# Kernel optimization log

Measured on AMD Instinct MI355X. Metric: run time of the kernel, lower is better.

Reference implementation:

```python
import jax, jax.numpy as jnp
import numpy as np
import math

EPS = 1e-6

def _std(x, axis=None, keepdims=False):
    # torch.std default: unbiased (ddof=1)
    return jnp.std(x, axis=axis, keepdims=keepdims, ddof=1)

def setup_inputs() -> dict:
    key = jax.random.key(0)
    L = 2048
    inputs = jax.random.normal(key, (L,), dtype=jnp.float32)
    return {"inputs": inputs, "freq": 7}

def reference(inputs, freq):
    L = inputs.shape[0]
    t = jnp.linspace(-1.0, 1.0, L)
    phi = (2.0 * math.pi * freq) * t  # [L]

    # ---- coarse Lattice Lock search over 10x20x20x20 Gielis topologies ----
    m_grid = jnp.arange(1, 11, dtype=jnp.float32)             # [10]
    n1_grid = jnp.logspace(-1.0, 1.0, 20)                      # [20]
    n2_grid = jnp.logspace(-1.0, 1.0, 20)
    n3_grid = jnp.logspace(-1.0, 1.0, 20)

    M = m_grid[:, None, None, None, None]
    N1 = n1_grid[None, :, None, None, None]
    N2 = n2_grid[None, None, :, None, None]
    N3 = n3_grid[None, None, None, :, None]
    P = phi[None, None, None, None, :]                          # [1,1,1,1,L]

    # Gielis superformula projection: R = (|cos(m*phi/4)|^n2 + |sin(m*phi/4)|^n3)^(-1/n1)
    ang = M * P / 4.0                                           # [10,1,1,1,L] -> bcast
    ghost = (jnp.abs(jnp.cos(ang)) ** N2 + jnp.abs(jnp.sin(ang)) ** N3) ** (-1.0 / N1)
    ghost = ghost * jnp.sin(P)                                  # [10,20,20,20,L]
    ghost = (ghost - ghost.mean(-1, keepdims=True)) / (_std(ghost, -1, True) + EPS)

    target = (inputs - inputs.mean()) / (_std(inputs) + EPS)    # [L]

    mse = jnp.mean((ghost - target) ** 2, axis=-1)              # [10,20,20,20]
    mi, i1, i2, i3 = jnp.unravel_index(jnp.argmin(mse), mse.shape)
    c_m = m_grid[mi]
    c_n1 = n1_grid[i1]
    c_n2 = n2_grid[i2]
    c_n3 = n3_grid[i3]

    # ---- fine search 30x30x30 around coarse optimum (m fixed) ----
    n1_f = jnp.linspace(c_n1 * 0.8, c_n1 * 1.2, 30)
    n2_f = jnp.linspace(c_n2 * 0.8, c_n2 * 1.2, 30)
    n3_f = jnp.linspace(c_n3 * 0.8, c_n3 * 1.2, 30)
    N1_F = n1_f[:, None, None, None]
    N2_F = n2_f[None, :, None, None]
    N3_F = n3_f[None, None, :, None]
    PHI_F = phi[None, None, None, :]

    ang_f = c_m * PHI_F / 4.0
    R_f = (jnp.abs(jnp.cos(ang_f)) ** N2_F + jnp.abs(jnp.sin(ang_f)) ** N3_F) ** (-1.0 / N1_F)
    S_f = R_f * jnp.sin(PHI_F)                                  # [30,30,30,L]
    S_f = (S_f - S_f.mean(-1, keepdims=True)) / (_std(S_f, -1, True) + EPS)

    mse_f = jnp.mean((S_f - target) ** 2, axis=-1)              # [30,30,30]
    f1, f2, f3 = jnp.unravel_index(jnp.argmin(mse_f), mse_f.shape)

    return jnp.stack([c_m, n1_f[f1], n2_f[f2], n3_f[f3]])
```

## Files before the change

### kernel.cpp

```cpp
#include <hip/hip_runtime.h>

#define L    2048
#define HALF 1024
#define NM   10
#define NG   20
#define NF   30

#define NCC2 2000
#define NFC2 450

#define OFF_SC   0
#define OFF_TAB  2048
#define OFF_G20  (2048 + 2*NM*HALF)
#define OFF_R20  (OFF_G20 + 20)
#define OFF_DWS  (OFF_R20 + 20)

#define EXP2F(x) __builtin_amdgcn_exp2f(x)
#define LOG2F(x) __builtin_amdgcn_logf(x)

typedef float f32x2 __attribute__((ext_vector_type(2)));

__device__ __forceinline__ f32x2 pk_mul(f32x2 a, f32x2 b) { return a * b; }
__device__ __forceinline__ f32x2 pk_fma(f32x2 a, f32x2 b, f32x2 c) {
  return __builtin_elementwise_fma(a, b, c);
}
__device__ __forceinline__ f32x2 pk_exp2(f32x2 v) {
  f32x2 e; e.x = EXP2F(v.x); e.y = EXP2F(v.y); return e;
}

__device__ __forceinline__ float grid20(int i) {
  double e = -1.0 + 2.0 * (double)i / 19.0;
  return (float)exp2(e * 3.3219280948873623478703194294894);
}
__device__ __forceinline__ float finev(float c, int j) {
  return (float)((double)c * 0.8 + (double)j * ((double)c * 0.4 / 29.0));
}
__device__ __forceinline__ double mse_from(double sgg2, double sgt, double sum_tt) {
  double S = sgg2; if (S < 0.0) S = 0.0;
  double d = sqrt(S / (double)(L - 1)) + 1e-6;
  return (S / (d * d) - 2.0 * sgt / d + sum_tt) / (double)L;
}
__device__ __forceinline__ void vt_wave_reduce(double& v, int& t) {
  for (int o = 32; o > 0; o >>= 1) {
    double ov = __shfl_down(v, o);
    int ot = __shfl_down(t, o);
    if (ov < v || (ov == v && ot < t)) { v = ov; t = ot; }
  }
}
__device__ __forceinline__ void vt_block_merge(double& v, int& t, double* sv, int* st) {
  int lane = threadIdx.x & 63, w = threadIdx.x >> 6;
  vt_wave_reduce(v, t);
  if (lane == 0) { sv[w] = v; st[w] = t; }
  __syncthreads();
  if (threadIdx.x == 0) {
    for (int k = 1; k < 4; k++)
      if (sv[k] < v || (sv[k] == v && st[k] < t)) { v = sv[k]; t = st[k]; }
  }
}

__global__ __launch_bounds__(256) void k_init(const float* __restrict__ x,
                                              const int* __restrict__ freqp,
                                              float* __restrict__ fws,
                                              double* __restrict__ dstt) {
  if (blockIdx.x == 0) {
    int tid = threadIdx.x;
    int lane = tid & 63, w = tid >> 6;
    __shared__ double sh[8];
    __shared__ double s_mean, s_d;

    double sx = 0.0, sxx = 0.0;
    for (int l = tid; l < L; l += 256) {
      double v = (double)x[l];
      sx += v; sxx += v * v;
    }
    for (int o = 32; o > 0; o >>= 1) { sx += __shfl_down(sx, o); sxx += __shfl_down(sxx, o); }
    if (lane == 0) { sh[w] = sx; sh[4 + w] = sxx; }
    __syncthreads();
    if (tid == 0) {
      sx = sh[0] + sh[1] + sh[2] + sh[3];
      sxx = sh[4] + sh[5] + sh[6] + sh[7];
      double mean = sx / (double)L;
      double S = sxx - sx * sx / (double)L; if (S < 0.0) S = 0.0;
      s_mean = mean; s_d = sqrt(S / (double)(L - 1)) + 1e-6;
    }
    __syncthreads();
    double mean = s_mean, d = s_d;
    double freq = (double)freqp[0];

    double stt = 0.0;
    for (int l = tid; l < HALF; l += 256) {
      float tva = (float)(((double)x[l] - mean) / d);
      float tvb = (float)(((double)x[L - 1 - l] - mean) / d);
      float tdv = tva - tvb;
      double t = -1.0 + 2.0 * (double)l / 2047.0;
      float spv = (float)sin(6.2831853071795864769 * freq * t);
      float2 scv; scv.x = spv * spv; scv.y = spv * tdv;
      reinterpret_cast<float2*>(fws + OFF_SC)[l] = scv;
      stt += (double)tva * (double)tva + (double)tvb * (double)tvb;
    }
    for (int o = 32; o > 0; o >>= 1) { stt += __shfl_down(stt, o); }
    __syncthreads();
    if (lane == 0) { sh[w] = stt; }
    __syncthreads();
    if (tid == 0) { dstt[0] = sh[0] + sh[1] + sh[2] + sh[3]; }
  } else {
    int l = (blockIdx.x - 1) * 256 + threadIdx.x;
    double freq = (double)freqp[0];
    double t = -1.0 + 2.0 * (double)l / 2047.0;
    double theta = 6.2831853071795864769 * freq * t * 0.25;
    double s1, c1;
    sincos(theta, &s1, &c1);
    double sk = s1, ck = c1;
    float2* tabp = reinterpret_cast<float2*>(fws + OFF_TAB);
#pragma unroll
    for (int m = 0; m < NM; ++m) {
      float2 v;
      v.x = fmaxf(LOG2F(fabsf((float)ck)), -1.0e4f);
      v.y = fmaxf(LOG2F(fabsf((float)sk)), -1.0e4f);
      tabp[m * HALF + l] = v;
      double sn = sk * c1 + ck * s1;
      double cn = ck * c1 - sk * s1;
      sk = sn; ck = cn;
    }
    if (blockIdx.x == 1 && threadIdx.x < NG) {
      float g = grid20(threadIdx.x);
      fws[OFF_G20 + threadIdx.x] = g;
      fws[OFF_R20 + threadIdx.x] = -1.0f / g;
    }
  }
}

__global__ __launch_bounds__(256) void k_coarse(const float* __restrict__ fws,
                                                const double* __restrict__ dstt,
                                                double* __restrict__ bv,
                                                int* __restrict__ bt) {
  __shared__ float4 row_ls[512];
  __shared__ float4 row_sc[512];
  __shared__ float2 cells[40];
  __shared__ int cellt[40];
  int tid = threadIdx.x, lane = tid & 63, w = tid >> 6;
  int b = blockIdx.x;
  int m = b / 200;
  int rem = b % 200;
  int i2 = rem / 10;
  int p3 = rem % 10;
  int i3A = 2 * p3;
  float n2 = fws[OFF_G20 + i2];
  float n3A = fws[OFF_G20 + i3A];
  float n3B = fws[OFF_G20 + i3A + 1];

  const float2* tab = reinterpret_cast<const float2*>(fws + OFF_TAB) + m * HALF;
  const float2* sc = reinterpret_cast<const float2*>(fws + OFF_SC);
#pragma unroll
  for (int k = 0; k < 2; k++) {
    int q = tid + k * 256;
    int e0 = 2 * q, e1 = e0 + 1;
    float2 tb0 = tab[e0], tb1 = tab[e1];
    float2 s0 = sc[e0], s1 = sc[e1];
    float a20 = EXP2F(n2 * tb0.x), a21 = EXP2F(n2 * tb1.x);
    float4 ls;
    ls.x = LOG2F(a20 + EXP2F(n3A * tb0.y));
    ls.y = LOG2F(a21 + EXP2F(n3A * tb1.y));
    ls.z = LOG2F(a20 + EXP2F(n3B * tb0.y));
    ls.w = LOG2F(a21 + EXP2F(n3B * tb1.y));
    row_ls[q] = ls;
    row_sc[q] = make_float4(s0.x, s1.x, s0.y, s1.y);
  }
  __syncthreads();

#pragma unroll
  for (int pass = 0; pass < 3; ++pass) {
    const bool two = (pass < 2);
    int i1a = w * 5 + pass * 2;
    float r0s = fws[OFF_R20 + i1a];
    float r1s = two ? fws[OFF_R20 + i1a + 1] : 0.0f;
    f32x2 r0 = {r0s, r0s}, r1 = {r1s, r1s};
    f32x2 z = {0.0f, 0.0f};
    f32x2 aA0 = z, tA0 = z, aB0 = z, tB0 = z;
    f32x2 aA1 = z, tA1 = z, aB1 = z, tB1 = z;
#pragma unroll 4
    for (int it = 0; it < 8; ++it) {
      int q = lane + it * 64;
      float4 ls4 = row_ls[q];
      float4 sc4 = row_sc[q];
      f32x2 lsA = {ls4.x, ls4.y}, lsB = {ls4.z, ls4.w};
      f32x2 sx = {sc4.x, sc4.y}, sy = {sc4.z, sc4.w};
      f32x2 e, e2;
      e = pk_exp2(pk_mul(r0, lsA)); e2 = pk_mul(e, e);
      aA0 = pk_fma(e2, sx, aA0); tA0 = pk_fma(e, sy, tA0);
      e = pk_exp2(pk_mul(r0, lsB)); e2 = pk_mul(e, e);
      aB0 = pk_fma(e2, sx, aB0); tB0 = pk_fma(e, sy, tB0);
      if (two) {
        e = pk_exp2(pk_mul(r1, lsA)); e2 = pk_mul(e, e);
        aA1 = pk_fma(e2, sx, aA1); tA1 = pk_fma(e, sy, tA1);
        e = pk_exp2(pk_mul(r1, lsB)); e2 = pk_mul(e, e);
        aB1 = pk_fma(e2, sx, aB1); tB1 = pk_fma(e, sy, tB1);
      }
    }
    float aA0s = aA0.x + aA0.y, tA0s = tA0.x + tA0.y;
    float aB0s = aB0.x + aB0.y, tB0s = tB0.x + tB0.y;
    float aA1s = aA1.x + aA1.y, tA1s = tA1.x + tA1.y;
    float aB1s = aB1.x + aB1.y, tB1s = tB1.x + tB1.y;
    for (int o = 32; o > 0; o >>= 1) {
      aA0s += __shfl_down(aA0s, o); tA0s += __shfl_down(tA0s, o);
      aB0s += __shfl_down(aB0s, o); tB0s += __shfl_down(tB0s, o);
      if (two) {
        aA1s += __shfl_down(aA1s, o); tA1s += __shfl_down(tA1s, o);
        aB1s += __shfl_down(aB1s, o); tB1s += __shfl_down(tB1s, o);
      }
    }
    if (lane == 0) {
      int t0 = ((m * NG + i1a) * NG + i2) * NG + i3A;
      int s0 = w * 10 + pass * 4;
      cells[s0]     = make_float2(aA0s, tA0s); cellt[s0]     = t0;
      cells[s0 + 1] = make_float2(aB0s, tB0s); cellt[s0 + 1] = t0 + 1;
      if (two) {
        cells[s0 + 2] = make_float2(aA1s, tA1s); cellt[s0 + 2] = t0 + NG * NG;
        cells[s0 + 3] = make_float2(aB1s, tB1s); cellt[s0 + 3] = t0 + NG * NG + 1;
      }
    }
  }
  __syncthreads();

  if (w == 0) {
    double v = 1e300; int t = 0x7fffffff;
    if (lane < 40) {
      float2 p = cells[lane];
      v = mse_from(2.0 * (double)p.x, (double)p.y, dstt[0]);
      t = cellt[lane];
    }
    vt_wave_reduce(v, t);
    if (lane == 0) { bv[b] = v; bt[b] = t; }
  }
}

__global__ __launch_bounds__(256) void k_fine(const float* __restrict__ fws,
                                              const double* __restrict__ dstt,
                                              const double* __restrict__ bvc,
                                              const int* __restrict__ btc,
                                              double* __restrict__ bvf,
                                              int* __restrict__ btf) {
  __shared__ float4 row_ls[512];
  __shared__ float4 row_sc[512];
  __shared__ float2 cells[60];
  __shared__ int cellt[60];
  __shared__ double sv[4];
  __shared__ int st[4];
  __shared__ float s_cn[4];
  {
    double v = 1e300; int t = 0x7fffffff;
    for (int i = threadIdx.x; i < NCC2; i += 256) {
      double ov = bvc[i]; int ot = btc[i];
      if (ov < v || (ov == v && ot < t)) { v = ov; t = ot; }
    }
    vt_block_merge(v, t, sv, st);
    if (threadIdx.x == 0) {
      int ci = t;
      int m  = ci / (NG * NG * NG);
      int rr = ci % (NG * NG * NG);
      s_cn[0] = grid20(rr / (NG * NG));
      s_cn[1] = grid20((rr / NG) % NG);
      s_cn[2] = grid20(rr % NG);
      s_cn[3] = (float)m;
    }
  }
  __syncthreads();
  float cn1 = s_cn[0], cn2 = s_cn[1], cn3 = s_cn[2];
  int m = (int)s_cn[3];

  int tid = threadIdx.x, lane = tid & 63, w = tid >> 6;
  int b = blockIdx.x;
  int j2 = b / 15;
  int p3 = b % 15;
  int j3A = 2 * p3;
  float n2 = finev(cn2, j2);
  float n3A = finev(cn3, j3A);
  float n3B = finev(cn3, j3A + 1);

  const float2* tab = reinterpret_cast<const float2*>(fws + OFF_TAB) + m * HALF;
  const float2* sc = reinterpret_cast<const float2*>(fws + OFF_SC);
#pragma unroll
  for (int k = 0; k < 2; k++) {
    int q = tid + k * 256;
    int e0 = 2 * q, e1 = e0 + 1;
    float2 tb0 = tab[e0], tb1 = tab[e1];
    float2 s0 = sc[e0], s1 = sc[e1];
    float a20 = EXP2F(n2 * tb0.x), a21 = EXP2F(n2 * tb1.x);
    float4 ls;
    ls.x = LOG2F(a20 + EXP2F(n3A * tb0.y));
    ls.y = LOG2F(a21 + EXP2F(n3A * tb1.y));
    ls.z = LOG2F(a20 + EXP2F(n3B * tb0.y));
    ls.w = LOG2F(a21 + EXP2F(n3B * tb1.y));
    row_ls[q] = ls;
    row_sc[q] = make_float4(s0.x, s1.x, s0.y, s1.y);
  }
  __syncthreads();

  int npairs = (w < 3) ? 4 : 3;
  for (int pp = 0; pp < npairs; ++pp) {
    int j1a = w * 8 + pp * 2;
    float r0s = -1.0f / finev(cn1, j1a);
    float r1s = -1.0f / finev(cn1, j1a + 1);
    f32x2 r0 = {r0s, r0s}, r1 = {r1s, r1s};
    f32x2 z = {0.0f, 0.0f};
    f32x2 aA0 = z, tA0 = z, aB0 = z, tB0 = z;
    f32x2 aA1 = z, tA1 = z, aB1 = z, tB1 = z;
#pragma unroll 4
    for (int it = 0; it < 8; ++it) {
      int q = lane + it * 64;
      float4 ls4 = row_ls[q];
      float4 sc4 = row_sc[q];
      f32x2 lsA = {ls4.x, ls4.y}, lsB = {ls4.z, ls4.w};
      f32x2 sx = {sc4.x, sc4.y}, sy = {sc4.z, sc4.w};
      f32x2 e, e2;
      e = pk_exp2(pk_mul(r0, lsA)); e2 = pk_mul(e, e);
      aA0 = pk_fma(e2, sx, aA0); tA0 = pk_fma(e, sy, tA0);
      e = pk_exp2(pk_mul(r0, lsB)); e2 = pk_mul(e, e);
      aB0 = pk_fma(e2, sx, aB0); tB0 = pk_fma(e, sy, tB0);
      e = pk_exp2(pk_mul(r1, lsA)); e2 = pk_mul(e, e);
      aA1 = pk_fma(e2, sx, aA1); tA1 = pk_fma(e, sy, tA1);
      e = pk_exp2(pk_mul(r1, lsB)); e2 = pk_mul(e, e);
      aB1 = pk_fma(e2, sx, aB1); tB1 = pk_fma(e, sy, tB1);
    }
    float aA0s = aA0.x + aA0.y, tA0s = tA0.x + tA0.y;
    float aB0s = aB0.x + aB0.y, tB0s = tB0.x + tB0.y;
    float aA1s = aA1.x + aA1.y, tA1s = tA1.x + tA1.y;
    float aB1s = aB1.x + aB1.y, tB1s = tB1.x + tB1.y;
    for (int o = 32; o > 0; o >>= 1) {
      aA0s += __shfl_down(aA0s, o); tA0s += __shfl_down(tA0s, o);
      aB0s += __shfl_down(aB0s, o); tB0s += __shfl_down(tB0s, o);
      aA1s += __shfl_down(aA1s, o); tA1s += __shfl_down(tA1s, o);
      aB1s += __shfl_down(aB1s, o); tB1s += __shfl_down(tB1s, o);
    }
    if (lane == 0) {
      int t0 = (j1a * NF + j2) * NF + j3A;
      int s0 = w * 16 + pp * 4;
      cells[s0]     = make_float2(aA0s, tA0s); cellt[s0]     = t0;
      cells[s0 + 1] = make_float2(aB0s, tB0s); cellt[s0 + 1] = t0 + 1;
      cells[s0 + 2] = make_float2(aA1s, tA1s); cellt[s0 + 2] = t0 + NF * NF;
      cells[s0 + 3] = make_float2(aB1s, tB1s); cellt[s0 + 3] = t0 + NF * NF + 1;
    }
  }
  __syncthreads();

  if (w == 0) {
    double v = 1e300; int t = 0x7fffffff;
    if (lane < 60) {
      float2 p = cells[lane];
      v = mse_from(2.0 * (double)p.x, (double)p.y, dstt[0]);
      t = cellt[lane];
    }
    vt_wave_reduce(v, t);
    if (lane == 0) { bvf[b] = v; btf[b] = t; }
  }
}

__global__ __launch_bounds__(256) void k_out(const double* __restrict__ bvc,
                                             const int* __restrict__ btc,
                                             const double* __restrict__ bvf,
                                             const int* __restrict__ btf,
                                             float* __restrict__ out) {
  __shared__ double sv[4];
  __shared__ int st[4];
  __shared__ int s_ci;
  {
    double v = 1e300; int t = 0x7fffffff;
    for (int i = threadIdx.x; i < NCC2; i += 256) {
      double ov = bvc[i]; int ot = btc[i];
      if (ov < v || (ov == v && ot < t)) { v = ov; t = ot; }
    }
    vt_block_merge(v, t, sv, st);
    if (threadIdx.x == 0) s_ci = t;
  }
  __syncthreads();
  {
    double v = 1e300; int t = 0x7fffffff;
    for (int i = threadIdx.x; i < NFC2; i += 256) {
      double ov = bvf[i]; int ot = btf[i];
      if (ov < v || (ov == v && ot < t)) { v = ov; t = ot; }
    }
    vt_block_merge(v, t, sv, st);
    if (threadIdx.x == 0) {
      int ci = s_ci;
      int m  = ci / (NG * NG * NG);
      int rr = ci % (NG * NG * NG);
      float cn1 = grid20(rr / (NG * NG));
      float cn2 = grid20((rr / NG) % NG);
      float cn3 = grid20(rr % NG);
      int fi = t;
      int f1 = fi / (NF * NF);
      int fc = fi % (NF * NF);
      out[0] = (float)(m + 1);
      out[1] = finev(cn1, f1);
      out[2] = finev(cn2, fc / NF);
      out[3] = finev(cn3, fc % NF);
    }
  }
}

extern "C" void kernel_launch(void* const* d_in, const int* in_sizes, int n_in,
                              void* d_out, int out_size, void* d_ws, size_t ws_size,
                              hipStream_t stream) {
  const float* x = (const float*)d_in[0];
  const int* freqp = (const int*)d_in[1];
  float* out = (float*)d_out;
  float* fws = (float*)d_ws;

  double* D0  = (double*)(fws + OFF_DWS);
  double* dstt = D0;
  double* bvc = D0 + 1;
  double* bvf = bvc + NCC2;
  int* btc = (int*)(bvf + NFC2);
  int* btf = btc + NCC2;

  hipLaunchKernelGGL(k_init,   dim3(5),    dim3(256), 0, stream, x, freqp, fws, dstt);
  hipLaunchKernelGGL(k_coarse, dim3(NCC2), dim3(256), 0, stream, fws, dstt, bvc, btc);
  hipLaunchKernelGGL(k_fine,   dim3(NFC2), dim3(256), 0, stream, fws, dstt, bvc, btc, bvf, btf);
  hipLaunchKernelGGL(k_out,    dim3(1),    dim3(256), 0, stream, bvc, btc, bvf, btf, out);
}
```

Measured before the change: 50.48 us.

## Split fine search along L across blocks and keep sin coefficients in registers

The sin²/sin·target coefficients are stored pre-interleaved as float4 and loaded straight into registers in both search kernels, which removes the shared-memory row_sc staging array. The fine-search kernel is split in half along the sample dimension, so twice as many blocks run and each computes half the log table. Partial sums go to a global buffer, and a new k_ffin kernel combines the halves, computes the MSE and does a first-level argmin. This aims to fill more CUs in the fine stage and to cut LDS traffic, at the cost of an extra kernel launch and global partial writes.

```diff
diff --git a/kernel.cpp b/kernel.cpp
--- a/kernel.cpp
+++ b/kernel.cpp
@@ -7,9 +7,10 @@
 #define NF   30
 
 #define NCC2 2000
-#define NFC2 450
-
-#define OFF_SC   0
+#define NFB2 900
+#define NBF  106
+
+#define OFF_SCP  0
 #define OFF_TAB  2048
 #define OFF_G20  (2048 + 2*NM*HALF)
 #define OFF_R20  (OFF_G20 + 20)
@@ -94,8 +95,8 @@
       float tdv = tva - tvb;
       double t = -1.0 + 2.0 * (double)l / 2047.0;
       float spv = (float)sin(6.2831853071795864769 * freq * t);
-      float2 scv; scv.x = spv * spv; scv.y = spv * tdv;
-      reinterpret_cast<float2*>(fws + OFF_SC)[l] = scv;
+      fws[OFF_SCP + (l >> 1) * 4 + (l & 1)]     = spv * spv;
+      fws[OFF_SCP + (l >> 1) * 4 + 2 + (l & 1)] = spv * tdv;
       stt += (double)tva * (double)tva + (double)tvb * (double)tvb;
     }
     for (int o = 32; o > 0; o >>= 1) { stt += __shfl_down(stt, o); }
@@ -135,7 +136,6 @@
                                                 double* __restrict__ bv,
                                                 int* __restrict__ bt) {
   __shared__ float4 row_ls[512];
-  __shared__ float4 row_sc[512];
   __shared__ float2 cells[40];
   __shared__ int cellt[40];
   int tid = threadIdx.x, lane = tid & 63, w = tid >> 6;
@@ -150,13 +150,11 @@
   float n3B = fws[OFF_G20 + i3A + 1];
 
   const float2* tab = reinterpret_cast<const float2*>(fws + OFF_TAB) + m * HALF;
-  const float2* sc = reinterpret_cast<const float2*>(fws + OFF_SC);
 #pragma unroll
   for (int k = 0; k < 2; k++) {
     int q = tid + k * 256;
     int e0 = 2 * q, e1 = e0 + 1;
     float2 tb0 = tab[e0], tb1 = tab[e1];
-    float2 s0 = sc[e0], s1 = sc[e1];
     float a20 = EXP2F(n2 * tb0.x), a21 = EXP2F(n2 * tb1.x);
     float4 ls;
     ls.x = LOG2F(a20 + EXP2F(n3A * tb0.y));
@@ -164,8 +162,17 @@
     ls.z = LOG2F(a20 + EXP2F(n3B * tb0.y));
     ls.w = LOG2F(a21 + EXP2F(n3B * tb1.y));
     row_ls[q] = ls;
-    row_sc[q] = make_float4(s0.x, s1.x, s0.y, s1.y);
-  }
+  }
+
+  const float4* scp4 = reinterpret_cast<const float4*>(fws + OFF_SCP);
+  float4 s_0 = scp4[lane];
+  float4 s_1 = scp4[lane + 64];
+  float4 s_2 = scp4[lane + 128];
+  float4 s_3 = scp4[lane + 192];
+  float4 s_4 = scp4[lane + 256];
+  float4 s_5 = scp4[lane + 320];
+  float4 s_6 = scp4[lane + 384];
+  float4 s_7 = scp4[lane + 448];
   __syncthreads();
 
 #pragma unroll
@@ -178,25 +185,28 @@
     f32x2 z = {0.0f, 0.0f};
     f32x2 aA0 = z, tA0 = z, aB0 = z, tB0 = z;
     f32x2 aA1 = z, tA1 = z, aB1 = z, tB1 = z;
-#pragma unroll 4
-    for (int it = 0; it < 8; ++it) {
-      int q = lane + it * 64;
-      float4 ls4 = row_ls[q];
-      float4 sc4 = row_sc[q];
-      f32x2 lsA = {ls4.x, ls4.y}, lsB = {ls4.z, ls4.w};
-      f32x2 sx = {sc4.x, sc4.y}, sy = {sc4.z, sc4.w};
-      f32x2 e, e2;
-      e = pk_exp2(pk_mul(r0, lsA)); e2 = pk_mul(e, e);
-      aA0 = pk_fma(e2, sx, aA0); tA0 = pk_fma(e, sy, tA0);
-      e = pk_exp2(pk_mul(r0, lsB)); e2 = pk_mul(e, e);
-      aB0 = pk_fma(e2, sx, aB0); tB0 = pk_fma(e, sy, tB0);
-      if (two) {
-        e = pk_exp2(pk_mul(r1, lsA)); e2 = pk_mul(e, e);
-        aA1 = pk_fma(e2, sx, aA1); tA1 = pk_fma(e, sy, tA1);
-        e = pk_exp2(pk_mul(r1, lsB)); e2 = pk_mul(e, e);
-        aB1 = pk_fma(e2, sx, aB1); tB1 = pk_fma(e, sy, tB1);
-      }
-    }
+
+#define C_IT(IT, SCV) do {                                         \
+    float4 ls4 = row_ls[lane + IT * 64];                           \
+    f32x2 lsA = {ls4.x, ls4.y}, lsB = {ls4.z, ls4.w};              \
+    f32x2 sx = {SCV.x, SCV.y}, sy = {SCV.z, SCV.w};                \
+    f32x2 e, e2;                                                   \
+    e = pk_exp2(pk_mul(r0, lsA)); e2 = pk_mul(e, e);               \
+    aA0 = pk_fma(e2, sx, aA0); tA0 = pk_fma(e, sy, tA0);           \
+    e = pk_exp2(pk_mul(r0, lsB)); e2 = pk_mul(e, e);               \
+    aB0 = pk_fma(e2, sx, aB0); tB0 = pk_fma(e, sy, tB0);           \
+    if (two) {                                                     \
+      e = pk_exp2(pk_mul(r1, lsA)); e2 = pk_mul(e, e);             \
+      aA1 = pk_fma(e2, sx, aA1); tA1 = pk_fma(e, sy, tA1);         \
+      e = pk_exp2(pk_mul(r1, lsB)); e2 = pk_mul(e, e);             \
+      aB1 = pk_fma(e2, sx, aB1); tB1 = pk_fma(e, sy, tB1);         \
+    }                                                              \
+  } while (0)
+
+    C_IT(0, s_0); C_IT(1, s_1); C_IT(2, s_2); C_IT(3, s_3);
+    C_IT(4, s_4); C_IT(5, s_5); C_IT(6, s_6); C_IT(7, s_7);
+#undef C_IT
+
     float aA0s = aA0.x + aA0.y, tA0s = tA0.x + tA0.y;
     float aB0s = aB0.x + aB0.y, tB0s = tB0.x + tB0.y;
     float aA1s = aA1.x + aA1.y, tA1s = tA1.x + tA1.y;
@@ -235,15 +245,10 @@
 }
 
 __global__ __launch_bounds__(256) void k_fine(const float* __restrict__ fws,
-                                              const double* __restrict__ dstt,
                                               const double* __restrict__ bvc,
                                               const int* __restrict__ btc,
-                                              double* __restrict__ bvf,
-                                              int* __restrict__ btf) {
-  __shared__ float4 row_ls[512];
-  __shared__ float4 row_sc[512];
-  __shared__ float2 cells[60];
-  __shared__ int cellt[60];
+                                              float2* __restrict__ partf) {
+  __shared__ float4 row_ls[256];
   __shared__ double sv[4];
   __shared__ int st[4];
   __shared__ float s_cn[4];
@@ -270,21 +275,20 @@
 
   int tid = threadIdx.x, lane = tid & 63, w = tid >> 6;
   int b = blockIdx.x;
-  int j2 = b / 15;
-  int p3 = b % 15;
+  int cp = b >> 1, ec = b & 1;
+  int j2 = cp / 15;
+  int p3 = cp % 15;
   int j3A = 2 * p3;
   float n2 = finev(cn2, j2);
   float n3A = finev(cn3, j3A);
   float n3B = finev(cn3, j3A + 1);
 
   const float2* tab = reinterpret_cast<const float2*>(fws + OFF_TAB) + m * HALF;
-  const float2* sc = reinterpret_cast<const float2*>(fws + OFF_SC);
-#pragma unroll
-  for (int k = 0; k < 2; k++) {
-    int q = tid + k * 256;
-    int e0 = 2 * q, e1 = e0 + 1;
+  {
+    int q = tid;
+    int gq = ec * 256 + q;
+    int e0 = 2 * gq, e1 = e0 + 1;
     float2 tb0 = tab[e0], tb1 = tab[e1];
-    float2 s0 = sc[e0], s1 = sc[e1];
     float a20 = EXP2F(n2 * tb0.x), a21 = EXP2F(n2 * tb1.x);
     float4 ls;
     ls.x = LOG2F(a20 + EXP2F(n3A * tb0.y));
@@ -292,8 +296,12 @@
     ls.z = LOG2F(a20 + EXP2F(n3B * tb0.y));
     ls.w = LOG2F(a21 + EXP2F(n3B * tb1.y));
     row_ls[q] = ls;
-    row_sc[q] = make_float4(s0.x, s1.x, s0.y, s1.y);
-  }
+  }
+  const float4* scp4 = reinterpret_cast<const float4*>(fws + OFF_SCP) + ec * 256;
+  float4 s_0 = scp4[lane];
+  float4 s_1 = scp4[lane + 64];
+  float4 s_2 = scp4[lane + 128];
+  float4 s_3 = scp4[lane + 192];
   __syncthreads();
 
   int npairs = (w < 3) ? 4 : 3;
@@ -305,23 +313,25 @@
     f32x2 z = {0.0f, 0.0f};
     f32x2 aA0 = z, tA0 = z, aB0 = z, tB0 = z;
     f32x2 aA1 = z, tA1 = z, aB1 = z, tB1 = z;
-#pragma unroll 4
-    for (int it = 0; it < 8; ++it) {
-      int q = lane + it * 64;
-      float4 ls4 = row_ls[q];
-      float4 sc4 = row_sc[q];
-      f32x2 lsA = {ls4.x, ls4.y}, lsB = {ls4.z, ls4.w};
-      f32x2 sx = {sc4.x, sc4.y}, sy = {sc4.z, sc4.w};
-      f32x2 e, e2;
-      e = pk_exp2(pk_mul(r0, lsA)); e2 = pk_mul(e, e);
-      aA0 = pk_fma(e2, sx, aA0); tA0 = pk_fma(e, sy, tA0);
-      e = pk_exp2(pk_mul(r0, lsB)); e2 = pk_mul(e, e);
-      aB0 = pk_fma(e2, sx, aB0); tB0 = pk_fma(e, sy, tB0);
-      e = pk_exp2(pk_mul(r1, lsA)); e2 = pk_mul(e, e);
-      aA1 = pk_fma(e2, sx, aA1); tA1 = pk_fma(e, sy, tA1);
-      e = pk_exp2(pk_mul(r1, lsB)); e2 = pk_mul(e, e);
-      aB1 = pk_fma(e2, sx, aB1); tB1 = pk_fma(e, sy, tB1);
-    }
+
+#define F_IT(IT, SCV) do {                                         \
+    float4 ls4 = row_ls[lane + IT * 64];                           \
+    f32x2 lsA = {ls4.x, ls4.y}, lsB = {ls4.z, ls4.w};              \
+    f32x2 sx = {SCV.x, SCV.y}, sy = {SCV.z, SCV.w};                \
+    f32x2 e, e2;                                                   \
+    e = pk_exp2(pk_mul(r0, lsA)); e2 = pk_mul(e, e);               \
+    aA0 = pk_fma(e2, sx, aA0); tA0 = pk_fma(e, sy, tA0);           \
+    e = pk_exp2(pk_mul(r0, lsB)); e2 = pk_mul(e, e);               \
+    aB0 = pk_fma(e2, sx, aB0); tB0 = pk_fma(e, sy, tB0);           \
+    e = pk_exp2(pk_mul(r1, lsA)); e2 = pk_mul(e, e);               \
+    aA1 = pk_fma(e2, sx, aA1); tA1 = pk_fma(e, sy, tA1);           \
+    e = pk_exp2(pk_mul(r1, lsB)); e2 = pk_mul(e, e);               \
+    aB1 = pk_fma(e2, sx, aB1); tB1 = pk_fma(e, sy, tB1);           \
+  } while (0)
+
+    F_IT(0, s_0); F_IT(1, s_1); F_IT(2, s_2); F_IT(3, s_3);
+#undef F_IT
+
     float aA0s = aA0.x + aA0.y, tA0s = tA0.x + tA0.y;
     float aB0s = aB0.x + aB0.y, tB0s = tB0.x + tB0.y;
     float aA1s = aA1.x + aA1.y, tA1s = tA1.x + tA1.y;
@@ -334,31 +344,39 @@
     }
     if (lane == 0) {
       int t0 = (j1a * NF + j2) * NF + j3A;
-      int s0 = w * 16 + pp * 4;
-      cells[s0]     = make_float2(aA0s, tA0s); cellt[s0]     = t0;
-      cells[s0 + 1] = make_float2(aB0s, tB0s); cellt[s0 + 1] = t0 + 1;
-      cells[s0 + 2] = make_float2(aA1s, tA1s); cellt[s0 + 2] = t0 + NF * NF;
-      cells[s0 + 3] = make_float2(aB1s, tB1s); cellt[s0 + 3] = t0 + NF * NF + 1;
-    }
-  }
-  __syncthreads();
-
-  if (w == 0) {
-    double v = 1e300; int t = 0x7fffffff;
-    if (lane < 60) {
-      float2 p = cells[lane];
-      v = mse_from(2.0 * (double)p.x, (double)p.y, dstt[0]);
-      t = cellt[lane];
-    }
-    vt_wave_reduce(v, t);
-    if (lane == 0) { bvf[b] = v; btf[b] = t; }
-  }
+      partf[2 * t0 + ec]       = make_float2(aA0s, tA0s);
+      partf[2 * (t0 + 1) + ec] = make_float2(aB0s, tB0s);
+      int t1 = t0 + NF * NF;
+      partf[2 * t1 + ec]       = make_float2(aA1s, tA1s);
+      partf[2 * (t1 + 1) + ec] = make_float2(aB1s, tB1s);
+    }
+  }
+}
+
+__global__ __launch_bounds__(256) void k_ffin(const float2* __restrict__ partf,
+                                              const double* __restrict__ dstt,
+                                              double* __restrict__ pv,
+                                              int* __restrict__ pi) {
+  int t = blockIdx.x * 256 + threadIdx.x;
+  double best = 1e300; int bi = 0x7fffffff;
+  if (t < NF * NF * NF) {
+    float2 p0 = partf[2 * t];
+    float2 p1 = partf[2 * t + 1];
+    double sgg = (double)p0.x + (double)p1.x;
+    double sgt = (double)p0.y + (double)p1.y;
+    best = mse_from(2.0 * sgg, sgt, dstt[0]);
+    bi = t;
+  }
+  __shared__ double sv[4];
+  __shared__ int st[4];
+  vt_block_merge(best, bi, sv, st);
+  if (threadIdx.x == 0) { pv[blockIdx.x] = best; pi[blockIdx.x] = bi; }
 }
 
 __global__ __launch_bounds__(256) void k_out(const double* __restrict__ bvc,
                                              const int* __restrict__ btc,
-                                             const double* __restrict__ bvf,
-                                             const int* __restrict__ btf,
+                                             const double* __restrict__ pvf,
+                                             const int* __restrict__ pif,
                                              float* __restrict__ out) {
   __shared__ double sv[4];
   __shared__ int st[4];
@@ -375,8 +393,8 @@
   __syncthreads();
   {
     double v = 1e300; int t = 0x7fffffff;
-    for (int i = threadIdx.x; i < NFC2; i += 256) {
-      double ov = bvf[i]; int ot = btf[i];
+    for (int i = threadIdx.x; i < NBF; i += 256) {
+      double ov = pvf[i]; int ot = pif[i];
       if (ov < v || (ov == v && ot < t)) { v = ov; t = ot; }
     }
     vt_block_merge(v, t, sv, st);
@@ -409,12 +427,14 @@
   double* D0  = (double*)(fws + OFF_DWS);
   double* dstt = D0;
   double* bvc = D0 + 1;
-  double* bvf = bvc + NCC2;
-  int* btc = (int*)(bvf + NFC2);
-  int* btf = btc + NCC2;
+  double* pvf = bvc + NCC2;
+  int* btc = (int*)(pvf + NBF);
+  int* pif = btc + NCC2;
+  float2* partf = (float2*)(pif + NBF + 1);
 
   hipLaunchKernelGGL(k_init,   dim3(5),    dim3(256), 0, stream, x, freqp, fws, dstt);
   hipLaunchKernelGGL(k_coarse, dim3(NCC2), dim3(256), 0, stream, fws, dstt, bvc, btc);
-  hipLaunchKernelGGL(k_fine,   dim3(NFC2), dim3(256), 0, stream, fws, dstt, bvc, btc, bvf, btf);
-  hipLaunchKernelGGL(k_out,    dim3(1),    dim3(256), 0, stream, bvc, btc, bvf, btf, out);
-}
+  hipLaunchKernelGGL(k_fine,   dim3(NFB2), dim3(256), 0, stream, fws, bvc, btc, partf);
+  hipLaunchKernelGGL(k_ffin,   dim3(NBF),  dim3(256), 0, stream, partf, dstt, pvf, pif);
+  hipLaunchKernelGGL(k_out,    dim3(1),    dim3(256), 0, stream, bvc, btc, pvf, pif, out);
+}
```

Result: slower. 53.30 us (+5.6%).

## Split fine search across signal halves and separate coarse-min into own kernel

Applied to the files above, without the earlier changes.

The fine-search kernel previously ran 450 blocks, each redoing the 2000-entry coarse argmin and covering the whole signal. A single-block k_cmin now computes the coarse optimum once and stores it in the workspace. k_fine then runs 900 blocks, each handling half the signal, and writes per-cell partial sums that a new k_ffin kernel combines before the final argmin. This gives more blocks to fill the GPU and removes redundant reductions, at the cost of two extra launches and a global round trip for the partial sums.

```diff
diff --git a/kernel.cpp b/kernel.cpp
--- a/kernel.cpp
+++ b/kernel.cpp
@@ -7,13 +7,15 @@
 #define NF   30
 
 #define NCC2 2000
-#define NFC2 450
+#define NFB2 900
+#define NBF  106
 
 #define OFF_SC   0
 #define OFF_TAB  2048
 #define OFF_G20  (2048 + 2*NM*HALF)
 #define OFF_R20  (OFF_G20 + 20)
-#define OFF_DWS  (OFF_R20 + 20)
+#define OFF_CN   (OFF_R20 + 20)
+#define OFF_DWS  (OFF_CN + 4)
 
 #define EXP2F(x) __builtin_amdgcn_exp2f(x)
 #define LOG2F(x) __builtin_amdgcn_logf(x)
@@ -234,44 +236,42 @@
   }
 }
 
-__global__ __launch_bounds__(256) void k_fine(const float* __restrict__ fws,
-                                              const double* __restrict__ dstt,
-                                              const double* __restrict__ bvc,
+__global__ __launch_bounds__(256) void k_cmin(const double* __restrict__ bvc,
                                               const int* __restrict__ btc,
-                                              double* __restrict__ bvf,
-                                              int* __restrict__ btf) {
-  __shared__ float4 row_ls[512];
-  __shared__ float4 row_sc[512];
-  __shared__ float2 cells[60];
-  __shared__ int cellt[60];
+                                              float* __restrict__ fws) {
   __shared__ double sv[4];
   __shared__ int st[4];
-  __shared__ float s_cn[4];
-  {
-    double v = 1e300; int t = 0x7fffffff;
-    for (int i = threadIdx.x; i < NCC2; i += 256) {
-      double ov = bvc[i]; int ot = btc[i];
-      if (ov < v || (ov == v && ot < t)) { v = ov; t = ot; }
-    }
-    vt_block_merge(v, t, sv, st);
-    if (threadIdx.x == 0) {
-      int ci = t;
-      int m  = ci / (NG * NG * NG);
-      int rr = ci % (NG * NG * NG);
-      s_cn[0] = grid20(rr / (NG * NG));
-      s_cn[1] = grid20((rr / NG) % NG);
-      s_cn[2] = grid20(rr % NG);
-      s_cn[3] = (float)m;
-    }
-  }
-  __syncthreads();
-  float cn1 = s_cn[0], cn2 = s_cn[1], cn3 = s_cn[2];
-  int m = (int)s_cn[3];
-
+  double v = 1e300; int t = 0x7fffffff;
+  for (int i = threadIdx.x; i < NCC2; i += 256) {
+    double ov = bvc[i]; int ot = btc[i];
+    if (ov < v || (ov == v && ot < t)) { v = ov; t = ot; }
+  }
+  vt_block_merge(v, t, sv, st);
+  if (threadIdx.x == 0) {
+    int ci = t;
+    int m  = ci / (NG * NG * NG);
+    int rr = ci % (NG * NG * NG);
+    fws[OFF_CN + 0] = grid20(rr / (NG * NG));
+    fws[OFF_CN + 1] = grid20((rr / NG) % NG);
+    fws[OFF_CN + 2] = grid20(rr % NG);
+    fws[OFF_CN + 3] = (float)m;
+  }
+}
+
+__global__ __launch_bounds__(256) void k_fine(const float* __restrict__ fws,
+                                              float2* __restrict__ partf) {
+  __shared__ float4 row_ls[256];
+  __shared__ float4 row_sc[256];
   int tid = threadIdx.x, lane = tid & 63, w = tid >> 6;
+  float cn1 = fws[OFF_CN + 0];
+  float cn2 = fws[OFF_CN + 1];
+  float cn3 = fws[OFF_CN + 2];
+  int m = (int)fws[OFF_CN + 3];
+
   int b = blockIdx.x;
-  int j2 = b / 15;
-  int p3 = b % 15;
+  int cp = b >> 1, ec = b & 1;
+  int j2 = cp / 15;
+  int p3 = cp % 15;
   int j3A = 2 * p3;
   float n2 = finev(cn2, j2);
   float n3A = finev(cn3, j3A);
@@ -279,10 +279,10 @@
 
   const float2* tab = reinterpret_cast<const float2*>(fws + OFF_TAB) + m * HALF;
   const float2* sc = reinterpret_cast<const float2*>(fws + OFF_SC);
-#pragma unroll
-  for (int k = 0; k < 2; k++) {
-    int q = tid + k * 256;
-    int e0 = 2 * q, e1 = e0 + 1;
+  {
+    int q = tid;
+    int gq = ec * 256 + q;
+    int e0 = 2 * gq, e1 = e0 + 1;
     float2 tb0 = tab[e0], tb1 = tab[e1];
     float2 s0 = sc[e0], s1 = sc[e1];
     float a20 = EXP2F(n2 * tb0.x), a21 = EXP2F(n2 * tb1.x);
@@ -306,7 +306,7 @@
     f32x2 aA0 = z, tA0 = z, aB0 = z, tB0 = z;
     f32x2 aA1 = z, tA1 = z, aB1 = z, tB1 = z;
 #pragma unroll 4
-    for (int it = 0; it < 8; ++it) {
+    for (int it = 0; it < 4; ++it) {
       int q = lane + it * 64;
       float4 ls4 = row_ls[q];
       float4 sc4 = row_sc[q];
@@ -334,67 +334,59 @@
     }
     if (lane == 0) {
       int t0 = (j1a * NF + j2) * NF + j3A;
-      int s0 = w * 16 + pp * 4;
-      cells[s0]     = make_float2(aA0s, tA0s); cellt[s0]     = t0;
-      cells[s0 + 1] = make_float2(aB0s, tB0s); cellt[s0 + 1] = t0 + 1;
-      cells[s0 + 2] = make_float2(aA1s, tA1s); cellt[s0 + 2] = t0 + NF * NF;
-      cells[s0 + 3] = make_float2(aB1s, tB1s); cellt[s0 + 3] = t0 + NF * NF + 1;
-    }
-  }
-  __syncthreads();
-
-  if (w == 0) {
-    double v = 1e300; int t = 0x7fffffff;
-    if (lane < 60) {
-      float2 p = cells[lane];
-      v = mse_from(2.0 * (double)p.x, (double)p.y, dstt[0]);
-      t = cellt[lane];
-    }
-    vt_wave_reduce(v, t);
-    if (lane == 0) { bvf[b] = v; btf[b] = t; }
-  }
-}
-
-__global__ __launch_bounds__(256) void k_out(const double* __restrict__ bvc,
-                                             const int* __restrict__ btc,
-                                             const double* __restrict__ bvf,
-                                             const int* __restrict__ btf,
+      partf[2 * t0 + ec]       = make_float2(aA0s, tA0s);
+      partf[2 * (t0 + 1) + ec] = make_float2(aB0s, tB0s);
+      int t1 = t0 + NF * NF;
+      partf[2 * t1 + ec]       = make_float2(aA1s, tA1s);
+      partf[2 * (t1 + 1) + ec] = make_float2(aB1s, tB1s);
+    }
+  }
+}
+
+__global__ __launch_bounds__(256) void k_ffin(const float2* __restrict__ partf,
+                                              const double* __restrict__ dstt,
+                                              double* __restrict__ pv,
+                                              int* __restrict__ pi) {
+  int t = blockIdx.x * 256 + threadIdx.x;
+  double best = 1e300; int bi = 0x7fffffff;
+  if (t < NF * NF * NF) {
+    float2 p0 = partf[2 * t];
+    float2 p1 = partf[2 * t + 1];
+    double sgg = (double)p0.x + (double)p1.x;
+    double sgt = (double)p0.y + (double)p1.y;
+    best = mse_from(2.0 * sgg, sgt, dstt[0]);
+    bi = t;
+  }
+  __shared__ double sv[4];
+  __shared__ int st[4];
+  vt_block_merge(best, bi, sv, st);
+  if (threadIdx.x == 0) { pv[blockIdx.x] = best; pi[blockIdx.x] = bi; }
+}
+
+__global__ __launch_bounds__(256) void k_out(const float* __restrict__ fws,
+                                             const double* __restrict__ pvf,
+                                             const int* __restrict__ pif,
                                              float* __restrict__ out) {
   __shared__ double sv[4];
   __shared__ int st[4];
-  __shared__ int s_ci;
-  {
-    double v = 1e300; int t = 0x7fffffff;
-    for (int i = threadIdx.x; i < NCC2; i += 256) {
-      double ov = bvc[i]; int ot = btc[i];
-      if (ov < v || (ov == v && ot < t)) { v = ov; t = ot; }
-    }
-    vt_block_merge(v, t, sv, st);
-    if (threadIdx.x == 0) s_ci = t;
-  }
-  __syncthreads();
-  {
-    double v = 1e300; int t = 0x7fffffff;
-    for (int i = threadIdx.x; i < NFC2; i += 256) {
-      double ov = bvf[i]; int ot = btf[i];
-      if (ov < v || (ov == v && ot < t)) { v = ov; t = ot; }
-    }
-    vt_block_merge(v, t, sv, st);
-    if (threadIdx.x == 0) {
-      int ci = s_ci;
-      int m  = ci / (NG * NG * NG);
-      int rr = ci % (NG * NG * NG);
-      float cn1 = grid20(rr / (NG * NG));
-      float cn2 = grid20((rr / NG) % NG);
-      float cn3 = grid20(rr % NG);
-      int fi = t;
-      int f1 = fi / (NF * NF);
-      int fc = fi % (NF * NF);
-      out[0] = (float)(m + 1);
-      out[1] = finev(cn1, f1);
-      out[2] = finev(cn2, fc / NF);
-      out[3] = finev(cn3, fc % NF);
-    }
+  double v = 1e300; int t = 0x7fffffff;
+  for (int i = threadIdx.x; i < NBF; i += 256) {
+    double ov = pvf[i]; int ot = pif[i];
+    if (ov < v || (ov == v && ot < t)) { v = ov; t = ot; }
+  }
+  vt_block_merge(v, t, sv, st);
+  if (threadIdx.x == 0) {
+    float cn1 = fws[OFF_CN + 0];
+    float cn2 = fws[OFF_CN + 1];
+    float cn3 = fws[OFF_CN + 2];
+    int m = (int)fws[OFF_CN + 3];
+    int fi = t;
+    int f1 = fi / (NF * NF);
+    int fc = fi % (NF * NF);
+    out[0] = (float)(m + 1);
+    out[1] = finev(cn1, f1);
+    out[2] = finev(cn2, fc / NF);
+    out[3] = finev(cn3, fc % NF);
   }
 }
 
@@ -409,12 +401,15 @@
   double* D0  = (double*)(fws + OFF_DWS);
   double* dstt = D0;
   double* bvc = D0 + 1;
-  double* bvf = bvc + NCC2;
-  int* btc = (int*)(bvf + NFC2);
-  int* btf = btc + NCC2;
+  double* pvf = bvc + NCC2;
+  int* btc = (int*)(pvf + NBF);
+  int* pif = btc + NCC2;
+  float2* partf = (float2*)(pif + NBF + 1);
 
   hipLaunchKernelGGL(k_init,   dim3(5),    dim3(256), 0, stream, x, freqp, fws, dstt);
   hipLaunchKernelGGL(k_coarse, dim3(NCC2), dim3(256), 0, stream, fws, dstt, bvc, btc);
-  hipLaunchKernelGGL(k_fine,   dim3(NFC2), dim3(256), 0, stream, fws, dstt, bvc, btc, bvf, btf);
-  hipLaunchKernelGGL(k_out,    dim3(1),    dim3(256), 0, stream, bvc, btc, bvf, btf, out);
-}
+  hipLaunchKernelGGL(k_cmin,   dim3(1),    dim3(256), 0, stream, bvc, btc, fws);
+  hipLaunchKernelGGL(k_fine,   dim3(NFB2), dim3(256), 0, stream, fws, partf);
+  hipLaunchKernelGGL(k_ffin,   dim3(NBF),  dim3(256), 0, stream, partf, dstt, pvf, pif);
+  hipLaunchKernelGGL(k_out,    dim3(1),    dim3(256), 0, stream, fws, pvf, pif, out);
+}
```

Measured after the change: 51.21 us. No clear change (+1.5%).
